# Kernel optimization log

Measured on AMD Instinct MI355X. Metric: run time of the kernel, lower is better.

## Reference

```python
import jax, jax.numpy as jnp
import numpy as np

# Model dims (match init_kwargs / input_specs)
B, L, D = 4, 1024, 512
CHI, S = 32, 4          # bond_dim, spatial_bond_dim
TRUNC_THR = 1e-4        # relative SVD truncation threshold
LN_EPS = 1e-6


def setup_inputs() -> dict:
    key = jax.random.key(0)
    ks = jax.random.split(key, 6)
    def dense(k, fi, fo):
        return jax.random.normal(k, (fi, fo), jnp.float32) / np.float32(np.sqrt(fi))
    return {
        "x": jax.random.normal(ks[0], (B, L, D), jnp.float32),
        "W_site": dense(ks[1], D, CHI * S * CHI),
        "b_site": jnp.zeros((CHI * S * CHI,), jnp.float32),
        "W_bridge": dense(ks[2], S * CHI, CHI),
        "b_bridge": jnp.zeros((CHI,), jnp.float32),
        "W_out": dense(ks[3], CHI, D),
        "b_out": jnp.zeros((D,), jnp.float32),
        "gamma": jnp.ones((D,), jnp.float32),
        "beta": jnp.zeros((D,), jnp.float32),
        "W_gate": dense(ks[4], D, D),
        "b_gate": jnp.zeros((D,), jnp.float32),
    }


def _mps_temporal_scan(x, site_weights):
    """Sequential O(L*chi^2) MPS scan with per-step SVD truncation.

    x: [B, L, D]; site_weights: [B, L, chi, s, chi].
    State h_t [B, chi] is the (normalized) left environment vector. Each step
    contracts the left vector (state + input injection from the first chi
    features, since initial_state is zeros) with the site tensor, truncates
    small singular values (relative threshold), and accumulates log-norms.
    Returns outputs [B, L, s*chi] and log_probs [B, L].
    """
    u_seq = jnp.transpose(x[:, :, :CHI], (1, 0, 2))            # [L, B, chi]
    A_seq = jnp.transpose(site_weights, (1, 0, 2, 3, 4))        # [L, B, chi, s, chi]

    def step(h, inp):
        A, u = inp                                              # [B,chi,s,chi], [B,chi]
        left = h + u                                            # input-driven left vector
        M = jnp.einsum('bl,blpr->bpr', left, A)                 # [B, s, chi]
        U, Sv, Vh = jnp.linalg.svd(M, full_matrices=False)      # Sv: [B, min(s,chi)]
        mask = (Sv >= TRUNC_THR * Sv[:, :1]).astype(M.dtype)    # relative truncation
        St = Sv * mask
        Mt = jnp.einsum('bik,bk,bkr->bir', U, St, Vh)           # truncated site matrix
        nrm = jnp.sqrt(jnp.sum(St * St, axis=-1) + 1e-12)       # Frobenius norm -> log prob
        v = jnp.sum(Mt, axis=1)                                 # contract physical index
        h_new = v / (jnp.linalg.norm(v, axis=-1, keepdims=True) + 1e-12)
        return h_new, (Mt.reshape(Mt.shape[0], -1), jnp.log(nrm))

    h0 = jnp.zeros((x.shape[0], CHI), x.dtype)                  # initial_state = zeros
    _, (outs, logp) = jax.lax.scan(step, h0, (A_seq, u_seq))
    return jnp.transpose(outs, (1, 0, 2)), jnp.transpose(logp, (1, 0))


def reference(x, W_site, b_site, W_bridge, b_bridge, W_out, b_out,
              gamma, beta, W_gate, b_gate):
    x = x.astype(jnp.float32)
    Bb, Ll = x.shape[0], x.shape[1]
    # site_tensor_proj: Dense(chi*s*chi) applied directly to inputs
    site_weights = (x @ W_site + b_site).reshape(Bb, Ll, CHI, S, CHI)
    outs, _logp = _mps_temporal_scan(x, site_weights)           # [B, L, s*chi]
    y = outs @ W_bridge + b_bridge                              # mps_bridge -> [B,L,chi]
    y = y @ W_out + b_out                                       # output_projection -> [B,L,D]
    # LayerNorm(eps=1e-6)
    mu = jnp.mean(y, axis=-1, keepdims=True)
    var = jnp.mean((y - mu) ** 2, axis=-1, keepdims=True)
    yn = (y - mu) * jax.lax.rsqrt(var + LN_EPS) * gamma + beta
    # gated residual
    gate = jax.nn.sigmoid(x @ W_gate + b_gate)
    return gate * yn + (1.0 - gate) * x
```

## Files before the change

kernel.cpp:

```cpp
#include <hip/hip_runtime.h>
#include <math.h>

#define B_   4
#define L_   1024
#define D_   512
#define CHI_ 32
#define S_   4
#define BT_  (B_ * L_)
#define NC_  2560
#define DPRE 8

__device__ __forceinline__ float readlane_f(float v, int l) {
    return __int_as_float(__builtin_amdgcn_readlane(__float_as_int(v), l));
}

__device__ __forceinline__ float bpermute_f(int byte_idx, float v) {
    return __int_as_float(__builtin_amdgcn_ds_bpermute(byte_idx, __float_as_int(v)));
}

template <int CTRL>
__device__ __forceinline__ float dpp_add(float x) {
    int y = __builtin_amdgcn_update_dpp(0, __float_as_int(x), CTRL, 0xf, 0xf, true);
    return x + __int_as_float(y);
}

__device__ __forceinline__ float reduce32_to_lane31(float x) {
    x = dpp_add<0x111>(x);
    x = dpp_add<0x112>(x);
    x = dpp_add<0x114>(x);
    x = dpp_add<0x118>(x);
    x = dpp_add<0x142>(x);
    return x;
}

__device__ __forceinline__ float octet_sum(float x) {
    x = dpp_add<0x111>(x);
    x = dpp_add<0x112>(x);
    x = dpp_add<0x114>(x);
    return x;
}

__global__ __launch_bounds__(256) void buildW_kernel(
    const float* __restrict__ Ws, const float* __restrict__ bs,
    const float* __restrict__ Wb, const float* __restrict__ Wg,
    const float* __restrict__ bg, float* __restrict__ Wcomb,
    float* __restrict__ biasC)
{
    const int tid = threadIdx.x;

    if (blockIdx.x == 512) {
        for (int f = tid; f < NC_; f += 256) {
            float acc;
            if (f < 1024) {
                const int q = f >> 8, rem = f & 255, i = rem >> 2, e = rem & 3;
                const int l = 4 * (i & 7) + e, r = (i >> 3) + 8 * q;
                const float* p = bs + l * 128 + r;
                acc = p[0] + p[32] + p[64] + p[96];
            } else if (f < 2048) {
                const int g = f - 1024, l = g >> 5, j = g & 31;
                acc = 0.f;
                for (int pr = 0; pr < 128; ++pr)
                    acc = fmaf(bs[l * 128 + pr], Wb[pr * 32 + j], acc);
            } else {
                acc = bg[f - 2048];
            }
            biasC[f] = acc;
        }
        return;
    }

    __shared__ float wsrow[4096];
    __shared__ float wbs[4096];

    const int d = blockIdx.x;
    #pragma unroll
    for (int i = 0; i < 16; ++i) {
        wsrow[i * 256 + tid] = Ws[(size_t)d * 4096 + i * 256 + tid];
        wbs[i * 256 + tid]   = Wb[i * 256 + tid];
    }
    __syncthreads();

    float* wrow = Wcomb + (size_t)d * NC_;

    #pragma unroll
    for (int ii = 0; ii < 4; ++ii) {
        const int f = ii * 256 + tid;
        const int q = f >> 8, rem = f & 255, i = rem >> 2, e = rem & 3;
        const int l = 4 * (i & 7) + e, r = (i >> 3) + 8 * q;
        const float* p = wsrow + l * 128 + r;
        wrow[f] = p[0] + p[32] + p[64] + p[96];
    }
    #pragma unroll
    for (int ii = 0; ii < 4; ++ii) {
        const int g = ii * 256 + tid;
        const int l = g >> 5, j = g & 31;
        float acc = 0.f;
        #pragma unroll 8
        for (int pr = 0; pr < 128; ++pr)
            acc = fmaf(wsrow[l * 128 + pr], wbs[pr * 32 + j], acc);
        wrow[1024 + g] = acc;
    }
    #pragma unroll
    for (int ii = 0; ii < 2; ++ii) {
        const int c = ii * 256 + tid;
        wrow[2048 + c] = Wg[(size_t)d * 512 + c];
    }
}

__device__ __forceinline__ void gemm_tile_body(
    const float* __restrict__ A, const float* __restrict__ Bm,
    const float* __restrict__ bias, float* __restrict__ C,
    int M, int N, int K, int m0, int n0,
    float (*As)[132], float (*Bs)[132])
{
    const int tid = threadIdx.x;
    const int tx = tid & 15;
    const int ty = tid >> 4;

    float acc[8][8] = {};

    for (int k0 = 0; k0 < K; k0 += 32) {
        #pragma unroll
        for (int p = 0; p < 4; ++p) {
            const int m = (tid >> 3) + 32 * p;
            const int k = (tid & 7) * 4;
            const float4 av = *(const float4*)(A + (size_t)(m0 + m) * K + k0 + k);
            As[k + 0][m] = av.x;
            As[k + 1][m] = av.y;
            As[k + 2][m] = av.z;
            As[k + 3][m] = av.w;
        }
        #pragma unroll
        for (int p = 0; p < 2; ++p) {
            const int k = (tid >> 4) + 16 * p;
            const int n = (tid & 15) * 8;
            const float* bp = Bm + (size_t)(k0 + k) * N + n0 + n;
            *(float4*)&Bs[k][n]     = *(const float4*)bp;
            *(float4*)&Bs[k][n + 4] = *(const float4*)(bp + 4);
        }
        __syncthreads();

        #pragma unroll
        for (int kk = 0; kk < 32; ++kk) {
            const float4 a0 = *(const float4*)&As[kk][ty * 8];
            const float4 a1 = *(const float4*)&As[kk][ty * 8 + 4];
            const float4 b0 = *(const float4*)&Bs[kk][tx * 8];
            const float4 b1 = *(const float4*)&Bs[kk][tx * 8 + 4];
            const float a[8] = {a0.x, a0.y, a0.z, a0.w, a1.x, a1.y, a1.z, a1.w};
            const float b[8] = {b0.x, b0.y, b0.z, b0.w, b1.x, b1.y, b1.z, b1.w};
            #pragma unroll
            for (int i = 0; i < 8; ++i)
                #pragma unroll
                for (int j = 0; j < 8; ++j)
                    acc[i][j] = fmaf(a[i], b[j], acc[i][j]);
        }
        __syncthreads();
    }

    const float4 bv0 = *(const float4*)&bias[n0 + tx * 8];
    const float4 bv1 = *(const float4*)&bias[n0 + tx * 8 + 4];
    #pragma unroll
    for (int i = 0; i < 8; ++i) {
        float* cp = C + (size_t)(m0 + ty * 8 + i) * N + n0 + tx * 8;
        float4 o0, o1;
        o0.x = acc[i][0] + bv0.x; o0.y = acc[i][1] + bv0.y;
        o0.z = acc[i][2] + bv0.z; o0.w = acc[i][3] + bv0.w;
        o1.x = acc[i][4] + bv1.x; o1.y = acc[i][5] + bv1.y;
        o1.z = acc[i][6] + bv1.z; o1.w = acc[i][7] + bv1.w;
        *(float4*)cp       = o0;
        *(float4*)(cp + 4) = o1;
    }
}

__global__ __launch_bounds__(256) void gemm_bias_kernel(
    const float* __restrict__ A, const float* __restrict__ Bm,
    const float* __restrict__ bias, float* __restrict__ C,
    int M, int N, int K)
{
    __shared__ float As[32][132];
    __shared__ float Bs[32][132];
    gemm_tile_body(A, Bm, bias, C, M, N, K,
                   blockIdx.y * 128, blockIdx.x * 128, As, Bs);
}

__global__ __launch_bounds__(256) void cvec_kernel(
    const float* __restrict__ Cc, const float* __restrict__ x,
    float* __restrict__ cBuf)
{
    const int tid  = threadIdx.x;
    const int lane = tid & 63;
    const int bt   = blockIdx.x * 4 + (tid >> 6);

    const float* base = Cc + (size_t)bt * NC_ + 4 * lane;
    float4 a0 = *(const float4*)(base + 0);
    float4 a1 = *(const float4*)(base + 256);
    float4 a2 = *(const float4*)(base + 512);
    float4 a3 = *(const float4*)(base + 768);

    const float u = x[(size_t)bt * D_ + (lane & 31)];
    const int idx0 = 16 * (lane & 7);
    const float u0 = bpermute_f(idx0 + 0,  u);
    const float u1 = bpermute_f(idx0 + 4,  u);
    const float u2 = bpermute_f(idx0 + 8,  u);
    const float u3 = bpermute_f(idx0 + 12, u);

    float p0 = fmaf(u3, a0.w, fmaf(u2, a0.z, fmaf(u1, a0.y, u0 * a0.x)));
    float p1 = fmaf(u3, a1.w, fmaf(u2, a1.z, fmaf(u1, a1.y, u0 * a1.x)));
    float p2 = fmaf(u3, a2.w, fmaf(u2, a2.z, fmaf(u1, a2.y, u0 * a2.x)));
    float p3 = fmaf(u3, a3.w, fmaf(u2, a3.z, fmaf(u1, a3.y, u0 * a3.x)));

    p0 = octet_sum(p0); p1 = octet_sum(p1);
    p2 = octet_sum(p2); p3 = octet_sum(p3);

    if ((lane & 7) == 7) {
        const int k = lane >> 3;
        float* cp = cBuf + (size_t)bt * 32 + k;
        cp[0]  = p0;
        cp[8]  = p1;
        cp[16] = p2;
        cp[24] = p3;
    }
}

__global__ __launch_bounds__(256) void fused_scan_gemm2_kernel(
    const float* __restrict__ x, const float* __restrict__ Wcomb,
    const float* __restrict__ biasC, float* __restrict__ Cc,
    const float* __restrict__ cBuf, float* __restrict__ wOut)
{
    __shared__ float As[32][132];
    __shared__ float Bs[32][132];

    if (blockIdx.x < 4) {
        const int tid = threadIdx.x;
        if (tid >= 64) return;
        const int b = blockIdx.x;

        const float* At = Cc + (size_t)b * L_ * NC_ + 4 * tid;
        const float* cb = cBuf + (size_t)b * L_ * 32 + (tid & 31);
        float*       wo = wOut + (size_t)b * L_ * 64 + tid;

        const int idx0 = 16 * (tid & 7);
        const int idxR = 32 * (tid & 7) + 28;
        const bool selA = (tid >> 3) & 1;
        const bool selB = (tid >> 4) & 1;

        float4 areg[DPRE][4];
        float  creg[DPRE];

        #pragma unroll
        for (int j = 0; j < DPRE; ++j) {
            const float* ap = At + (size_t)j * NC_;
            #pragma unroll
            for (int q = 0; q < 4; ++q) areg[j][q] = *(const float4*)(ap + 256 * q);
            creg[j] = cb[j * 32];
        }

        float w = 0.f;

        for (int t = 0; t < L_; t += DPRE) {
            #pragma unroll
            for (int j = 0; j < DPRE; ++j) {
                wo[(t + j) * 64] = w;

                float red = reduce32_to_lane31(w * w);

                const float wb0 = bpermute_f(idx0 + 0,  w);
                const float wb1 = bpermute_f(idx0 + 4,  w);
                const float wb2 = bpermute_f(idx0 + 8,  w);
                const float wb3 = bpermute_f(idx0 + 12, w);

                float p0, p1, p2, p3;
                {
                    const float4 a0 = areg[j][0], a1 = areg[j][1];
                    const float4 a2 = areg[j][2], a3 = areg[j][3];
                    p0 = fmaf(wb3, a0.w, fmaf(wb2, a0.z, fmaf(wb1, a0.y, wb0 * a0.x)));
                    p1 = fmaf(wb3, a1.w, fmaf(wb2, a1.z, fmaf(wb1, a1.y, wb0 * a1.x)));
                    p2 = fmaf(wb3, a2.w, fmaf(wb2, a2.z, fmaf(wb1, a2.y, wb0 * a2.x)));
                    p3 = fmaf(wb3, a3.w, fmaf(wb2, a3.z, fmaf(wb1, a3.y, wb0 * a3.x)));
                }

                p0 = octet_sum(p0);
                p1 = octet_sum(p1);
                p2 = octet_sum(p2);
                p3 = octet_sum(p3);

                const float m0 = bpermute_f(idxR, p0);
                const float m1 = bpermute_f(idxR, p1);
                const float m2 = bpermute_f(idxR, p2);
                const float m3 = bpermute_f(idxR, p3);
                const float t0 = selA ? m1 : m0;
                const float t1 = selA ? m3 : m2;
                const float m  = selB ? t1 : t0;

                const float n2 = readlane_f(red, 31);
                const float rn = rsqrtf(n2 + 1e-24f);
                w = fmaf(m, rn, creg[j]);

                int tn = t + j + DPRE;
                if (tn > L_ - 1) tn = L_ - 1;
                const float* ap = At + (size_t)tn * NC_;
                #pragma unroll
                for (int q = 0; q < 4; ++q) areg[j][q] = *(const float4*)(ap + 256 * q);
                creg[j] = cb[tn * 32];
            }
        }
        return;
    }

    const int g  = blockIdx.x - 4;
    const int m0 = (g / 12) * 128;
    const int n0 = 1024 + (g % 12) * 128;
    gemm_tile_body(x, Wcomb, biasC, Cc, BT_, NC_, D_, m0, n0, As, Bs);
}

__global__ __launch_bounds__(128) void phaseB_kernel(
    const float* __restrict__ Cc, const float* __restrict__ x,
    const float* __restrict__ wBuf, const float* __restrict__ bb,
    float* __restrict__ y1)
{
    __shared__ float lf[32];
    __shared__ float part[4][32];

    const int bt = blockIdx.x;
    const int tid = threadIdx.x;

    if (tid < 64) {
        const float wv = wBuf[(size_t)bt * 64 + tid];
        float red = reduce32_to_lane31(wv * wv);
        const float n2 = readlane_f(red, 31);
        const float rn = rsqrtf(n2 + 1e-24f);
        if (tid < 32)
            lf[tid] = fmaf(wv, rn, x[(size_t)bt * D_ + tid]);
    }
    __syncthreads();

    const int j = tid & 31, q = tid >> 5;
    const float* Gp = Cc + (size_t)bt * NC_ + 1024;
    float p = 0.f;
    #pragma unroll
    for (int i = 0; i < 8; ++i)
        p = fmaf(lf[8 * q + i], Gp[(8 * q + i) * 32 + j], p);
    part[q][j] = p;
    __syncthreads();

    if (tid < 32)
        y1[bt * 32 + tid] = part[0][tid] + part[1][tid] + part[2][tid]
                          + part[3][tid] + bb[tid];
}

__global__ __launch_bounds__(256) void epilogue_kernel(
    const float* __restrict__ x, const float* __restrict__ y1buf,
    const float* __restrict__ Wout, const float* __restrict__ bout,
    const float* __restrict__ gamma, const float* __restrict__ beta,
    const float* __restrict__ Cc, float* __restrict__ out)
{
    __shared__ float ys[32];
    __shared__ float red1[4], red2[4];

    const int bt = blockIdx.x;
    const int tid = threadIdx.x;

    if (tid < 32) ys[tid] = y1buf[bt * 32 + tid];
    __syncthreads();

    float yv[2];
    #pragma unroll
    for (int q = 0; q < 2; ++q) {
        const int d = tid + q * 256;
        float acc = bout[d];
        #pragma unroll
        for (int j = 0; j < 32; ++j)
            acc = fmaf(ys[j], Wout[j * D_ + d], acc);
        yv[q] = acc;
    }

    float s1 = yv[0] + yv[1];
    float s2 = yv[0] * yv[0] + yv[1] * yv[1];
    #pragma unroll
    for (int m = 1; m <= 32; m <<= 1) {
        s1 += __shfl_xor(s1, m);
        s2 += __shfl_xor(s2, m);
    }
    const int wid = tid >> 6;
    if ((tid & 63) == 0) { red1[wid] = s1; red2[wid] = s2; }
    __syncthreads();
    const float S1 = red1[0] + red1[1] + red1[2] + red1[3];
    const float S2 = red2[0] + red2[1] + red2[2] + red2[3];
    const float mu  = S1 * (1.f / (float)D_);
    const float var = S2 * (1.f / (float)D_) - mu * mu;
    const float rstd = rsqrtf(var + 1e-6f);

    #pragma unroll
    for (int q = 0; q < 2; ++q) {
        const int d = tid + q * 256;
        const size_t gi = (size_t)bt * D_ + d;
        const float yn = (yv[q] - mu) * rstd * gamma[d] + beta[d];
        const float z = Cc[(size_t)bt * NC_ + 2048 + d];
        const float g = 1.f / (1.f + expf(-z));
        const float xv = x[gi];
        out[gi] = g * yn + (1.f - g) * xv;
    }
}

extern "C" void kernel_launch(void* const* d_in, const int* in_sizes, int n_in,
                              void* d_out, int out_size, void* d_ws, size_t ws_size,
                              hipStream_t stream)
{
    const float* x        = (const float*)d_in[0];
    const float* W_site   = (const float*)d_in[1];
    const float* b_site   = (const float*)d_in[2];
    const float* W_bridge = (const float*)d_in[3];
    const float* b_bridge = (const float*)d_in[4];
    const float* W_out    = (const float*)d_in[5];
    const float* b_out    = (const float*)d_in[6];
    const float* gamma    = (const float*)d_in[7];
    const float* beta     = (const float*)d_in[8];
    const float* W_gate   = (const float*)d_in[9];
    const float* b_gate   = (const float*)d_in[10];
    float* out = (float*)d_out;

    float* ws = (float*)d_ws;
    float* Wcomb = ws;
    float* biasC = Wcomb + (size_t)512 * NC_;
    float* Cc    = biasC + NC_;
    float* cBuf  = Cc    + (size_t)BT_ * NC_;
    float* wBuf  = cBuf  + (size_t)BT_ * 32;
    float* y1    = wBuf  + (size_t)BT_ * 64;

    buildW_kernel<<<dim3(513), dim3(256), 0, stream>>>(
        W_site, b_site, W_bridge, W_gate, b_gate, Wcomb, biasC);

    gemm_bias_kernel<<<dim3(8, BT_ / 128), dim3(256), 0, stream>>>(
        x, Wcomb, biasC, Cc, BT_, NC_, D_);

    cvec_kernel<<<dim3(BT_ / 4), dim3(256), 0, stream>>>(Cc, x, cBuf);

    fused_scan_gemm2_kernel<<<dim3(4 + 12 * (BT_ / 128)), dim3(256), 0, stream>>>(
        x, Wcomb, biasC, Cc, cBuf, wBuf);

    phaseB_kernel<<<dim3(BT_), dim3(128), 0, stream>>>(
        Cc, x, wBuf, b_bridge, y1);

    epilogue_kernel<<<dim3(BT_), dim3(256), 0, stream>>>(
        x, y1, W_out, b_out, gamma, beta, Cc, out);
}
```

Measured before the change: 390.7 us.

## Drop cvec precompute by folding input into scan; fuse phaseB with epilogue

The scan now builds the left vector as normalized state plus the raw input and contracts that with the site matrix, instead of adding a precomputed input contraction after the step. This removes the cvec kernel and its buffer. The phaseB and epilogue kernels are merged into one 256-thread kernel, which also removes the y1 intermediate buffer. The trade-off is that the rsqrt normalization and the x load now sit on the serial scan's critical path before the bpermutes, where before they overlapped with the matrix contraction.

```diff
diff --git a/kernel.cpp b/kernel.cpp
--- a/kernel.cpp
+++ b/kernel.cpp
@@ -183,49 +183,10 @@
                    blockIdx.y * 128, blockIdx.x * 128, As, Bs);
 }
 
-__global__ __launch_bounds__(256) void cvec_kernel(
-    const float* __restrict__ Cc, const float* __restrict__ x,
-    float* __restrict__ cBuf)
-{
-    const int tid  = threadIdx.x;
-    const int lane = tid & 63;
-    const int bt   = blockIdx.x * 4 + (tid >> 6);
-
-    const float* base = Cc + (size_t)bt * NC_ + 4 * lane;
-    float4 a0 = *(const float4*)(base + 0);
-    float4 a1 = *(const float4*)(base + 256);
-    float4 a2 = *(const float4*)(base + 512);
-    float4 a3 = *(const float4*)(base + 768);
-
-    const float u = x[(size_t)bt * D_ + (lane & 31)];
-    const int idx0 = 16 * (lane & 7);
-    const float u0 = bpermute_f(idx0 + 0,  u);
-    const float u1 = bpermute_f(idx0 + 4,  u);
-    const float u2 = bpermute_f(idx0 + 8,  u);
-    const float u3 = bpermute_f(idx0 + 12, u);
-
-    float p0 = fmaf(u3, a0.w, fmaf(u2, a0.z, fmaf(u1, a0.y, u0 * a0.x)));
-    float p1 = fmaf(u3, a1.w, fmaf(u2, a1.z, fmaf(u1, a1.y, u0 * a1.x)));
-    float p2 = fmaf(u3, a2.w, fmaf(u2, a2.z, fmaf(u1, a2.y, u0 * a2.x)));
-    float p3 = fmaf(u3, a3.w, fmaf(u2, a3.z, fmaf(u1, a3.y, u0 * a3.x)));
-
-    p0 = octet_sum(p0); p1 = octet_sum(p1);
-    p2 = octet_sum(p2); p3 = octet_sum(p3);
-
-    if ((lane & 7) == 7) {
-        const int k = lane >> 3;
-        float* cp = cBuf + (size_t)bt * 32 + k;
-        cp[0]  = p0;
-        cp[8]  = p1;
-        cp[16] = p2;
-        cp[24] = p3;
-    }
-}
-
 __global__ __launch_bounds__(256) void fused_scan_gemm2_kernel(
     const float* __restrict__ x, const float* __restrict__ Wcomb,
     const float* __restrict__ biasC, float* __restrict__ Cc,
-    const float* __restrict__ cBuf, float* __restrict__ wOut)
+    float* __restrict__ wOut)
 {
     __shared__ float As[32][132];
     __shared__ float Bs[32][132];
@@ -236,7 +197,7 @@
         const int b = blockIdx.x;
 
         const float* At = Cc + (size_t)b * L_ * NC_ + 4 * tid;
-        const float* cb = cBuf + (size_t)b * L_ * 32 + (tid & 31);
+        const float* xr = x  + (size_t)b * L_ * D_ + (tid & 31);
         float*       wo = wOut + (size_t)b * L_ * 64 + tid;
 
         const int idx0 = 16 * (tid & 7);
@@ -245,14 +206,14 @@
         const bool selB = (tid >> 4) & 1;
 
         float4 areg[DPRE][4];
-        float  creg[DPRE];
+        float  xreg[DPRE];
 
         #pragma unroll
         for (int j = 0; j < DPRE; ++j) {
             const float* ap = At + (size_t)j * NC_;
             #pragma unroll
             for (int q = 0; q < 4; ++q) areg[j][q] = *(const float4*)(ap + 256 * q);
-            creg[j] = cb[j * 32];
+            xreg[j] = xr[(size_t)j * D_];
         }
 
         float w = 0.f;
@@ -263,20 +224,23 @@
                 wo[(t + j) * 64] = w;
 
                 float red = reduce32_to_lane31(w * w);
-
-                const float wb0 = bpermute_f(idx0 + 0,  w);
-                const float wb1 = bpermute_f(idx0 + 4,  w);
-                const float wb2 = bpermute_f(idx0 + 8,  w);
-                const float wb3 = bpermute_f(idx0 + 12, w);
+                const float n2 = readlane_f(red, 31);
+                const float rn = rsqrtf(n2 + 1e-24f);
+                const float lft = fmaf(w, rn, xreg[j]);
+
+                const float lb0 = bpermute_f(idx0 + 0,  lft);
+                const float lb1 = bpermute_f(idx0 + 4,  lft);
+                const float lb2 = bpermute_f(idx0 + 8,  lft);
+                const float lb3 = bpermute_f(idx0 + 12, lft);
 
                 float p0, p1, p2, p3;
                 {
                     const float4 a0 = areg[j][0], a1 = areg[j][1];
                     const float4 a2 = areg[j][2], a3 = areg[j][3];
-                    p0 = fmaf(wb3, a0.w, fmaf(wb2, a0.z, fmaf(wb1, a0.y, wb0 * a0.x)));
-                    p1 = fmaf(wb3, a1.w, fmaf(wb2, a1.z, fmaf(wb1, a1.y, wb0 * a1.x)));
-                    p2 = fmaf(wb3, a2.w, fmaf(wb2, a2.z, fmaf(wb1, a2.y, wb0 * a2.x)));
-                    p3 = fmaf(wb3, a3.w, fmaf(wb2, a3.z, fmaf(wb1, a3.y, wb0 * a3.x)));
+                    p0 = fmaf(lb3, a0.w, fmaf(lb2, a0.z, fmaf(lb1, a0.y, lb0 * a0.x)));
+                    p1 = fmaf(lb3, a1.w, fmaf(lb2, a1.z, fmaf(lb1, a1.y, lb0 * a1.x)));
+                    p2 = fmaf(lb3, a2.w, fmaf(lb2, a2.z, fmaf(lb1, a2.y, lb0 * a2.x)));
+                    p3 = fmaf(lb3, a3.w, fmaf(lb2, a3.z, fmaf(lb1, a3.y, lb0 * a3.x)));
                 }
 
                 p0 = octet_sum(p0);
@@ -290,18 +254,14 @@
                 const float m3 = bpermute_f(idxR, p3);
                 const float t0 = selA ? m1 : m0;
                 const float t1 = selA ? m3 : m2;
-                const float m  = selB ? t1 : t0;
-
-                const float n2 = readlane_f(red, 31);
-                const float rn = rsqrtf(n2 + 1e-24f);
-                w = fmaf(m, rn, creg[j]);
+                w = selB ? t1 : t0;
 
                 int tn = t + j + DPRE;
                 if (tn > L_ - 1) tn = L_ - 1;
                 const float* ap = At + (size_t)tn * NC_;
                 #pragma unroll
                 for (int q = 0; q < 4; ++q) areg[j][q] = *(const float4*)(ap + 256 * q);
-                creg[j] = cb[tn * 32];
+                xreg[j] = xr[(size_t)tn * D_];
             }
         }
         return;
@@ -313,13 +273,17 @@
     gemm_tile_body(x, Wcomb, biasC, Cc, BT_, NC_, D_, m0, n0, As, Bs);
 }
 
-__global__ __launch_bounds__(128) void phaseB_kernel(
+__global__ __launch_bounds__(256) void phaseB_epilogue_kernel(
     const float* __restrict__ Cc, const float* __restrict__ x,
     const float* __restrict__ wBuf, const float* __restrict__ bb,
-    float* __restrict__ y1)
+    const float* __restrict__ Wout, const float* __restrict__ bout,
+    const float* __restrict__ gamma, const float* __restrict__ beta,
+    float* __restrict__ out)
 {
     __shared__ float lf[32];
-    __shared__ float part[4][32];
+    __shared__ float part[8][32];
+    __shared__ float ys[32];
+    __shared__ float red1[4], red2[4];
 
     const int bt = blockIdx.x;
     const int tid = threadIdx.x;
@@ -334,33 +298,23 @@
     }
     __syncthreads();
 
-    const int j = tid & 31, q = tid >> 5;
-    const float* Gp = Cc + (size_t)bt * NC_ + 1024;
-    float p = 0.f;
-    #pragma unroll
-    for (int i = 0; i < 8; ++i)
-        p = fmaf(lf[8 * q + i], Gp[(8 * q + i) * 32 + j], p);
-    part[q][j] = p;
-    __syncthreads();
-
-    if (tid < 32)
-        y1[bt * 32 + tid] = part[0][tid] + part[1][tid] + part[2][tid]
-                          + part[3][tid] + bb[tid];
-}
-
-__global__ __launch_bounds__(256) void epilogue_kernel(
-    const float* __restrict__ x, const float* __restrict__ y1buf,
-    const float* __restrict__ Wout, const float* __restrict__ bout,
-    const float* __restrict__ gamma, const float* __restrict__ beta,
-    const float* __restrict__ Cc, float* __restrict__ out)
-{
-    __shared__ float ys[32];
-    __shared__ float red1[4], red2[4];
-
-    const int bt = blockIdx.x;
-    const int tid = threadIdx.x;
-
-    if (tid < 32) ys[tid] = y1buf[bt * 32 + tid];
+    {
+        const int j = tid & 31, q = tid >> 5;
+        const float* Gp = Cc + (size_t)bt * NC_ + 1024;
+        float p = 0.f;
+        #pragma unroll
+        for (int i = 0; i < 4; ++i)
+            p = fmaf(lf[4 * q + i], Gp[(4 * q + i) * 32 + j], p);
+        part[q][j] = p;
+    }
+    __syncthreads();
+
+    if (tid < 32) {
+        float s = bb[tid];
+        #pragma unroll
+        for (int q = 0; q < 8; ++q) s += part[q][tid];
+        ys[tid] = s;
+    }
     __syncthreads();
 
     float yv[2];
@@ -423,9 +377,7 @@
     float* Wcomb = ws;
     float* biasC = Wcomb + (size_t)512 * NC_;
     float* Cc    = biasC + NC_;
-    float* cBuf  = Cc    + (size_t)BT_ * NC_;
-    float* wBuf  = cBuf  + (size_t)BT_ * 32;
-    float* y1    = wBuf  + (size_t)BT_ * 64;
+    float* wBuf  = Cc    + (size_t)BT_ * NC_;
 
     buildW_kernel<<<dim3(513), dim3(256), 0, stream>>>(
         W_site, b_site, W_bridge, W_gate, b_gate, Wcomb, biasC);
@@ -433,14 +385,9 @@
     gemm_bias_kernel<<<dim3(8, BT_ / 128), dim3(256), 0, stream>>>(
         x, Wcomb, biasC, Cc, BT_, NC_, D_);
 
-    cvec_kernel<<<dim3(BT_ / 4), dim3(256), 0, stream>>>(Cc, x, cBuf);
-
     fused_scan_gemm2_kernel<<<dim3(4 + 12 * (BT_ / 128)), dim3(256), 0, stream>>>(
-        x, Wcomb, biasC, Cc, cBuf, wBuf);
-
-    phaseB_kernel<<<dim3(BT_), dim3(128), 0, stream>>>(
-        Cc, x, wBuf, b_bridge, y1);
-
-    epilogue_kernel<<<dim3(BT_), dim3(256), 0, stream>>>(
-        x, y1, W_out, b_out, gamma, beta, Cc, out);
-}
+        x, Wcomb, biasC, Cc, wBuf);
+
+    phaseB_epilogue_kernel<<<dim3(BT_), dim3(256), 0, stream>>>(
+        Cc, x, wBuf, b_bridge, W_out, b_out, gamma, beta, out);
+}
```

Result: no change. 396.8 us (+1.6%).
